# Kernel optimization log

Measured on AMD Instinct MI355X. Metric: run time of the kernel, lower is better.

Reference implementation:

```python
import jax, jax.numpy as jnp
import numpy as np

L, B, T, D, V = 4, 32, 512, 512, 1000


def setup_inputs() -> dict:
    key = jax.random.key(0)
    k0, k1, k2, k3, k4 = jax.random.split(key, 5)
    ids = jax.random.randint(k0, (B, T), 0, V)
    mask = jax.random.randint(k1, (B, T), 0, 2).astype(bool)  # True = valid token
    emb = jax.random.normal(k2, (V, D), dtype=jnp.float32) * 0.1
    W = jax.random.normal(k3, (L, D, 3 * D), dtype=jnp.float32) / np.float32(np.sqrt(D))
    v = jax.random.normal(k4, (L, 2, D), dtype=jnp.float32) * 0.1  # (v_f, v_r) per layer
    b = jnp.zeros((L, 2, D), dtype=jnp.float32)                    # (b_f, b_r) per layer
    return {"ids": ids, "mask": mask, "emb": emb, "W": W, "v": v, "b": b}


def _sru_layer(x, pad, Wl, vf, vr, bf, br):
    # x: [T,B,D] layer input; pad: [T,B,1] bool (True = padded step)
    Tn, Bn, Dn = x.shape
    U = jnp.einsum('tbd,de->tbe', x, Wl).reshape(Tn, Bn, 3, Dn)
    xt, fpre, rpre = U[:, :, 0], U[:, :, 1], U[:, :, 2]

    def step(c, inp):
        xt_t, fp_t, rp_t, x_t, pad_t = inp
        f = jax.nn.sigmoid(fp_t + vf * c + bf)
        r = jax.nn.sigmoid(rp_t + vr * c + br)
        c_new = f * c + (1.0 - f) * xt_t
        h = r * jnp.tanh(c_new) + (1.0 - r) * x_t  # highway (input_size==hidden_size)
        c_out = jnp.where(pad_t, c, c_new)          # padded step: keep state
        h = jnp.where(pad_t, 0.0, h)                # padded step: zero output
        return c_out, h

    c0 = jnp.zeros_like(x[0])  # zero initial hidden state, as in the torch code
    _, h = jax.lax.scan(step, c0, (xt, fpre, rpre, x, pad))
    return h  # [T,B,D]


def reference(ids, mask, emb, W, v, b):
    x = emb[ids]                       # CharEmbedder lookup: [B,T,D]
    x = jnp.transpose(x, (1, 0, 2))    # [T,B,D]  (permute(1,0,2))
    pad = (~mask).T[:, :, None]        # inverted_mask.T -> [T,B,1]
    for l in range(L):
        x = _sru_layer(x, pad, W[l], v[l, 0], v[l, 1], b[l, 0], b[l, 1])
    return jnp.transpose(x, (1, 0, 2))  # back to [B,T,D]
```

## Files before the change

kernel.cpp:

```cpp
#include <hip/hip_runtime.h>
#include <hip/hip_bf16.h>


#define LAYERS 4
#define BB 32
#define TT 512
#define DD 512
#define N3 1536
#define MROWS (TT * BB)
#define WPL ((size_t)DD * N3)
#define SB 32
#define LOG2E 1.4426950408889634f
#define TWOLOG2E 2.8853900817779268f

typedef unsigned short u16;
typedef unsigned int u32;
typedef _Float16 half8 __attribute__((ext_vector_type(8)));
typedef float f32x4 __attribute__((ext_vector_type(4)));

__device__ __forceinline__ float b2f(u16 u) {
  union { unsigned int i; float f; } x;
  x.i = ((unsigned int)u) << 16;
  return x.f;
}
__device__ __forceinline__ u16 f2h(float f) {
  _Float16 h = (_Float16)f;
  return *(u16*)&h;
}
__device__ __forceinline__ float h2f(u16 u) {
  _Float16 h;
  *(u16*)&h = u;
  return (float)h;
}
__device__ __forceinline__ float rcpf(float x) { return __builtin_amdgcn_rcpf(x); }
__device__ __forceinline__ float exp2f_(float x) { return __builtin_amdgcn_exp2f(x); }

__device__ __forceinline__ void async_ld16(const void* g, void* l) {
  __builtin_amdgcn_global_load_lds(
      (const __attribute__((address_space(1))) void*)g,
      (__attribute__((address_space(3))) void*)l, 16, 0, 0);
}
__device__ __forceinline__ void async_ld4(const void* g, void* l) {
  __builtin_amdgcn_global_load_lds(
      (const __attribute__((address_space(1))) void*)g,
      (__attribute__((address_space(3))) void*)l, 4, 0, 0);
}

__global__ void detect_kernel(const u16* __restrict__ emb_u,
                              const int* __restrict__ mask_i,
                              const int* __restrict__ ids_i,
                              int* __restrict__ flags) {
  __shared__ int cnt[3];
  __shared__ int zc;
  int tid = threadIdx.x;
  if (tid < 3) cnt[tid] = 0;
  if (tid == 0) zc = 0;
  __syncthreads();
  int bad = 0, zero_even = 0;
  for (int i = tid; i < 8192; i += 256) {
    u16 u = emb_u[i];
    unsigned e = (u >> 7) & 0xFF;
    if (e >= 0x8F) bad++;
    if ((i & 1) == 0 && u == 0) zero_even++;
  }
  if (bad) atomicAdd(&cnt[0], bad);
  if (zero_even) atomicAdd(&zc, zero_even);
  if (tid < 64) {
    unsigned vv = (unsigned)mask_i[tid];
    if (vv > 1u) atomicAdd(&cnt[1], 1);
  }
  if (tid < 256) {
    if (ids_i[2 * tid + 1] == 0) atomicAdd(&cnt[2], 1);
  }
  __syncthreads();
  if (tid == 0) {
    flags[0] = (cnt[0] > 64 || zc > 3000) ? 1 : 0;
    flags[1] = (cnt[1] > 0) ? 1 : 0;
    flags[2] = (cnt[2] >= 192) ? 1 : 0;
  }
}

__global__ __launch_bounds__(256)
void wprep_kernel(const void* __restrict__ W, u16* __restrict__ W16,
                  const int* __restrict__ flags) {
  __shared__ float tileW[32][33];
  int l = blockIdx.z;
  int k0 = blockIdx.x * 32;
  int n0 = blockIdx.y * 32;
  int tx = threadIdx.x & 31;
  int ty = threadIdx.x >> 5;
  int ff = flags[0];
  const float* Wf = (const float*)W + (size_t)l * WPL;
  const u16* Wb = (const u16*)W + (size_t)l * WPL;
  for (int kk = ty; kk < 32; kk += 8) {
    size_t off = (size_t)(k0 + kk) * N3 + n0 + tx;
    tileW[kk][tx] = ff ? Wf[off] : b2f(Wb[off]);
  }
  __syncthreads();
  u16* outP = W16 + (size_t)l * WPL;
  for (int nn = ty; nn < 32; nn += 8) {
    float x = tileW[tx][nn];
    outP[(size_t)(n0 + nn) * DD + k0 + tx] = f2h(x);
  }
}

__global__ void embed_kernel(const int* __restrict__ ids,
                             const void* __restrict__ emb,
                             u16* __restrict__ X16,
                             const int* __restrict__ flags) {
  int i = blockIdx.x * 256 + threadIdx.x;
  int d = i & (DD - 1);
  int tb = i >> 9;
  int b = tb & (BB - 1);
  int t = tb >> 5;
  int ii = b * TT + t;
  int id = flags[2] ? ids[2 * ii] : ids[ii];
  float val = flags[0] ? ((const float*)emb)[id * DD + d]
                       : b2f(((const u16*)emb)[id * DD + d]);
  X16[i] = f2h(val);
}

__global__ __launch_bounds__(256)
void gemm_kernel(const u16* __restrict__ X16, const u16* __restrict__ W16l,
                 const void* __restrict__ bvec, int layer,
                 const int* __restrict__ flags,
                 u16* __restrict__ U16, int row_base, int chunkM) {
  __shared__ u16 At[128][64];
  __shared__ u16 Bt[128][64];
  const int tid = threadIdx.x;
  const int row0 = blockIdx.x * 128;
  const int col0 = blockIdx.y * 128;
  const int lane = tid & 63, wave = tid >> 6;
  const int wm = (wave >> 1) * 64, wn = (wave & 1) * 64;
  const int m16 = lane & 15, quad = lane >> 4;
  const int isA = (wave < 2);
  const int rbase = (wave & 1) * 64;
  const int srow = lane >> 3;
  const int sseg = (lane & 7) ^ (srow & 7);

  f32x4 acc[4][4];
#pragma unroll
  for (int mi = 0; mi < 4; ++mi)
#pragma unroll
    for (int ni = 0; ni < 4; ++ni)
#pragma unroll
      for (int r = 0; r < 4; ++r) acc[mi][ni][r] = 0.f;

  const u16* srcBase = isA ? X16 : W16l;
  const int gbase = isA ? (row_base + row0 + rbase) : (col0 + rbase);

  for (int kv = 0; kv < 512; kv += 64) {
    __syncthreads();
    {
      const u16* src = srcBase + (size_t)(gbase + srow) * DD + kv + sseg * 8;
      u16(*dst)[64] = isA ? At : Bt;
#pragma unroll
      for (int i = 0; i < 8; ++i)
        async_ld16(src + (size_t)i * 8 * DD, &dst[rbase + i * 8][0]);
    }
    __syncthreads();

    half8 af[2][4], bfr[2][4];
#pragma unroll
    for (int kk = 0; kk < 2; ++kk)
#pragma unroll
      for (int i = 0; i < 4; ++i) {
        int ra = wm + i * 16 + m16;
        af[kk][i] = *(const half8*)&At[ra][((kk * 4 + quad) ^ (ra & 7)) * 8];
        int rb = wn + i * 16 + m16;
        bfr[kk][i] = *(const half8*)&Bt[rb][((kk * 4 + quad) ^ (rb & 7)) * 8];
      }
#pragma unroll
    for (int kk = 0; kk < 2; ++kk)
#pragma unroll
      for (int mi = 0; mi < 4; ++mi)
#pragma unroll
        for (int ni = 0; ni < 4; ++ni)
          acc[mi][ni] = __builtin_amdgcn_mfma_f32_16x16x32_f16(
              af[kk][mi], bfr[kk][ni], acc[mi][ni], 0, 0, 0);
  }

  const int ff = flags[0];
#pragma unroll
  for (int ni = 0; ni < 4; ++ni) {
    int cix = col0 + wn + ni * 16 + m16;
    int p = cix >> 9;
    int dd = cix & 511;
    float bias = 0.f;
    if (p > 0) {
      size_t bo = (size_t)layer * 2 * DD + (size_t)(p - 1) * DD + dd;
      bias = ff ? ((const float*)bvec)[bo] : b2f(((const u16*)bvec)[bo]);
    }
    u16* up = U16 + (size_t)p * chunkM * 512;
#pragma unroll
    for (int mi = 0; mi < 4; ++mi) {
      int r0 = row0 + wm + mi * 16 + quad * 4;
#pragma unroll
      for (int reg = 0; reg < 4; ++reg) {
        float val = acc[mi][ni][reg];
        val = (p == 0) ? val : -(val + bias) * LOG2E;
        up[(size_t)(r0 + reg) * 512 + dd] = f2h(val);
      }
    }
  }
}

template <int EMIT>
__global__ __launch_bounds__(448, 1)
void scan_kernel(const u16* __restrict__ U16, float* __restrict__ X,
                 u16* __restrict__ X16,
                 const void* __restrict__ mask_p, const void* __restrict__ vbase,
                 int layer, const int* __restrict__ flags,
                 float* __restrict__ carry, int t0, int nt, int chunkM) {
  __shared__ u16 bufA[2][2][SB][64];
  __shared__ u16 bufB[3][2][SB][64];
  __shared__ float ring[2][2][SB][64];
  __shared__ int msk[TT];
  const int tid = threadIdx.x;
  const int wave = tid >> 6, lane = tid & 63;
  const int idx0 = blockIdx.x * 64;
  const int b = idx0 >> 9;
  const int d0 = idx0 & 511;
  const int ff = flags[0], fm = flags[1];

  const int* mi_ = (const int*)mask_p + b * TT;
  const unsigned char* mb_ = (const unsigned char*)mask_p + b * TT;
  for (int i = tid; i < nt; i += 448) msk[i] = fm ? (int)mb_[t0 + i] : mi_[t0 + i];

  float vfs = 0.f, vrs = 0.f, c = 0.f;
  {
    int d = d0 + lane;
    size_t voff = (size_t)layer * 2 * DD;
    if (wave == 0) {
      float vf = ff ? ((const float*)vbase)[voff + d]
                    : b2f(((const u16*)vbase)[voff + d]);
      vfs = -vf * LOG2E;
      c = (t0 == 0) ? 0.f : carry[idx0 + lane];
    } else if (wave >= 1 && wave <= 4) {
      float vr = ff ? ((const float*)vbase)[voff + DD + d]
                    : b2f(((const u16*)vbase)[voff + DD + d]);
      vrs = -vr * LOG2E;
    }
  }

  const int nbuf = nt / SB;

  auto ld_pair = [&](const u16* rowS, const u16* rowS1, void* ldst) {
    const u32* a0 = (const u32*)rowS;
    const u32* a1 = (const u32*)rowS1;
    const u32* ga = (lane < 32) ? (a0 + lane) : (a1 + (lane - 32));
    async_ld4(ga, ldst);
  };

  auto produceA = [&](int k) {
    int ph = k & 1, tl = k * SB;
    const u16* p0 = U16 + ((size_t)tl * BB + b) * 512 + d0;
    const u16* p1 = p0 + (size_t)chunkM * 512;
#pragma unroll
    for (int s = 0; s < SB; s += 2)
      ld_pair(p0 + (size_t)s * BB * 512, p0 + (size_t)(s + 1) * BB * 512,
              &bufA[ph][0][s][0]);
#pragma unroll
    for (int s = 0; s < SB; s += 2)
      ld_pair(p1 + (size_t)s * BB * 512, p1 + (size_t)(s + 1) * BB * 512,
              &bufA[ph][1][s][0]);
  };
  auto produceB = [&](int k) {
    int ph = k % 3, tl = k * SB;
    const u16* p2 = U16 + 2 * (size_t)chunkM * 512 + ((size_t)tl * BB + b) * 512 + d0;
    const u16* xb = X16 + ((size_t)(t0 + tl) * BB + b) * DD + d0;
#pragma unroll
    for (int s = 0; s < SB; s += 2)
      ld_pair(p2 + (size_t)s * BB * 512, p2 + (size_t)(s + 1) * BB * 512,
              &bufB[ph][0][s][0]);
#pragma unroll
    for (int s = 0; s < SB; s += 2)
      ld_pair(xb + (size_t)s * BB * DD, xb + (size_t)(s + 1) * BB * DD,
              &bufB[ph][1][s][0]);
  };

  float* Xp = X + (size_t)b * TT * DD + d0 + lane;

  auto hphase = [&](int j, int hw) {
    int phc = j & 1, phb = j % 3;
    int sbase = hw * (SB / 4);
#pragma unroll
    for (int si = 0; si < SB / 4; ++si) {
      int s = sbase + si;
      float cprev = ring[phc][0][s][lane];
      float cn = ring[phc][1][s][lane];
      float rps = h2f(bufB[phb][0][s][lane]);
      float xin = h2f(bufB[phb][1][s][lane]);
      int m = msk[j * SB + s];
      float tr = exp2f_(fmaf(vrs, cprev, rps));
      float r = rcpf(1.f + tr);
      float e2 = exp2f_(cn * TWOLOG2E);
      float th = fmaf(-2.f, rcpf(e2 + 1.f), 1.f);
      float h = fmaf(r, th - xin, xin);
      float hout = (m == 0) ? 0.f : h;
      int tg = t0 + j * SB + s;
      if (EMIT)
        X16[((size_t)tg * BB + b) * DD + d0 + lane] = f2h(hout);
      else
        Xp[(size_t)tg * DD] = hout;
    }
  };

  if (wave == 5) produceA(0);
  if (wave == 6) produceB(0);

  for (int k = 0; k < nbuf; ++k) {
    __syncthreads();
    if (wave == 5) {
      if (k + 1 < nbuf) produceA(k + 1);
    } else if (wave == 6) {
      if (k + 1 < nbuf) produceB(k + 1);
    } else if (wave == 0) {
      int ph = k & 1;
#pragma unroll 8
      for (int s = 0; s < SB; ++s) {
        float xt = h2f(bufA[ph][0][s][lane]);
        float fps = h2f(bufA[ph][1][s][lane]);
        float t = exp2f_(fmaf(vfs, c, fps));
        float f = rcpf(1.f + t);
        float cn = fmaf(f, c - xt, xt);
        ring[ph][0][s][lane] = c;
        ring[ph][1][s][lane] = cn;
        c = (msk[k * SB + s] == 0) ? c : cn;
      }
    } else {
      if (k > 0) hphase(k - 1, wave - 1);
    }
  }
  __syncthreads();
  if (wave >= 1 && wave <= 4) hphase(nbuf - 1, wave - 1);
  if (wave == 0) carry[idx0 + lane] = c;
}

__global__ void sentinel_kernel(float* out) { out[threadIdx.x] = 12345.f; }

extern "C" void kernel_launch(void* const* d_in, const int* in_sizes, int n_in,
                              void* d_out, int out_size, void* d_ws, size_t ws_size,
                              hipStream_t stream) {
  const int* ids = (const int*)d_in[0];
  const void* mask = d_in[1];
  const void* emb = d_in[2];
  const void* W = d_in[3];
  const void* v = d_in[4];
  const void* bp = d_in[5];

  char* ws = (char*)d_ws;
  int* flags = (int*)ws;
  float* carry = (float*)(ws + 4096);
  const size_t offX16 = 69632;
  const size_t offW16 = offX16 + (size_t)MROWS * DD * 2;
  const size_t offU = offW16 + (size_t)LAYERS * WPL * 2;
  const size_t perT = (size_t)BB * N3 * 2;

  const int cand[4] = {512, 256, 128, 64};
  int chunkT = 0;
  for (int i = 0; i < 4; ++i) {
    if (ws_size >= offU + (size_t)cand[i] * perT) { chunkT = cand[i]; break; }
  }
  if (!chunkT) {
    sentinel_kernel<<<1, 256, 0, stream>>>((float*)d_out);
    return;
  }
  const int chunkM = chunkT * BB;

  u16* X16 = (u16*)(ws + offX16);
  u16* W16 = (u16*)(ws + offW16);
  u16* U16 = (u16*)(ws + offU);
  float* X = (float*)d_out;

  detect_kernel<<<1, 256, 0, stream>>>((const u16*)emb, (const int*)mask,
                                       (const int*)ids, flags);
  wprep_kernel<<<dim3(16, 48, 4), 256, 0, stream>>>(W, W16, flags);
  embed_kernel<<<MROWS * DD / 256, 256, 0, stream>>>(ids, emb, X16, flags);

  int nch = TT / chunkT;
  for (int l = 0; l < LAYERS; ++l) {
    const u16* W16l = W16 + (size_t)l * WPL;
    for (int ch = 0; ch < nch; ++ch) {
      int t0 = ch * chunkT;
      dim3 g(chunkT * BB / 128, N3 / 128);
      gemm_kernel<<<g, 256, 0, stream>>>(X16, W16l, bp, l, flags, U16,
                                         t0 * BB, chunkM);
      if (l < LAYERS - 1)
        scan_kernel<1><<<BB * DD / 64, 448, 0, stream>>>(U16, X, X16, mask, v, l,
                                                         flags, carry, t0, chunkT,
                                                         chunkM);
      else
        scan_kernel<0><<<BB * DD / 64, 448, 0, stream>>>(U16, X, X16, mask, v, l,
                                                         flags, carry, t0, chunkT,
                                                         chunkM);
    }
  }
}
```

Baseline: 353.0 us.

## Rewrite GEMM with 256x256 tiles, 8 waves and double-buffered async LDS pipeline

The projection GEMM moves from 128x128 tiles with 4 waves and two barriers per K step to 256x256 tiles with 8 waves. Global-to-LDS async loads are double-buffered and prefetched several stages ahead, with manual vmcnt waits and raw s_barrier calls, and MFMA priority is raised. Workgroup IDs are remapped across groups of 8 so neighbouring blocks share operands in cache. The aim is more reuse per tile and load latency hidden behind MFMA work. The costs are fewer blocks (risk of idle CUs when chunkM is small), hand-tuned wait counts that must match the issue order, and an nblk that is assumed divisible by 8.

```diff
diff --git a/kernel.cpp b/kernel.cpp
--- a/kernel.cpp
+++ b/kernel.cpp
@@ -17,6 +17,9 @@
 typedef unsigned int u32;
 typedef _Float16 half8 __attribute__((ext_vector_type(8)));
 typedef float f32x4 __attribute__((ext_vector_type(4)));
+
+#define SBAR() asm volatile("s_barrier" ::: "memory")
+#define WAITVM(n) asm volatile("s_waitcnt vmcnt(" n ")" ::: "memory")
 
 __device__ __forceinline__ float b2f(u16 u) {
   union { unsigned int i; float f; } x;
@@ -120,88 +123,121 @@
   X16[i] = f2h(val);
 }
 
-__global__ __launch_bounds__(256)
+__global__ __launch_bounds__(512, 2)
 void gemm_kernel(const u16* __restrict__ X16, const u16* __restrict__ W16l,
                  const void* __restrict__ bvec, int layer,
                  const int* __restrict__ flags,
-                 u16* __restrict__ U16, int row_base, int chunkM) {
-  __shared__ u16 At[128][64];
-  __shared__ u16 Bt[128][64];
+                 u16* __restrict__ U16, int row_base, int chunkM, int nblk) {
+  __shared__ u16 lds[2][2][2][8192];
   const int tid = threadIdx.x;
-  const int row0 = blockIdx.x * 128;
-  const int col0 = blockIdx.y * 128;
   const int lane = tid & 63, wave = tid >> 6;
-  const int wm = (wave >> 1) * 64, wn = (wave & 1) * 64;
+  const int wm = wave >> 2, wn = wave & 3;
   const int m16 = lane & 15, quad = lane >> 4;
-  const int isA = (wave < 2);
-  const int rbase = (wave & 1) * 64;
-  const int srow = lane >> 3;
-  const int sseg = (lane & 7) ^ (srow & 7);
-
-  f32x4 acc[4][4];
-#pragma unroll
-  for (int mi = 0; mi < 4; ++mi)
+
+  const int orig = blockIdx.x;
+  const int wg = (orig & 7) * (nblk >> 3) + (orig >> 3);
+  const int mt = wg / 6, nt = wg - mt * 6;
+
+  const int arow0 = row_base + mt * 256;
+  const int bcol0 = nt * 256;
+
+  const int srow = lane >> 2;
+  const int sq = (lane & 3) ^ (srow & 3);
+  const u16* pa = X16 + (size_t)(arow0 + wave * 32 + srow) * DD + sq * 8;
+  const u16* pb = W16l + (size_t)(bcol0 + wave * 32 + srow) * DD + sq * 8;
+  const int ldsblk = wave * 2 * 512;
+
+  auto stage = [&](int s) {
+    const int ts = s >> 2, hi = s & 3;
+    const int mat = hi & 1, kk = hi >> 1, db = ts & 1;
+    const u16* src = (mat ? pb : pa) + ts * 64 + kk * 32;
+    u16* dst = &lds[db][mat][kk][ldsblk];
+    async_ld16(src, dst);
+    async_ld16(src + (size_t)16 * DD, dst + 512);
+  };
+
+  f32x4 acc[8][4];
+#pragma unroll
+  for (int mi = 0; mi < 8; ++mi)
 #pragma unroll
     for (int ni = 0; ni < 4; ++ni)
 #pragma unroll
       for (int r = 0; r < 4; ++r) acc[mi][ni][r] = 0.f;
 
-  const u16* srcBase = isA ? X16 : W16l;
-  const int gbase = isA ? (row_base + row0 + rbase) : (col0 + rbase);
-
-  for (int kv = 0; kv < 512; kv += 64) {
-    __syncthreads();
-    {
-      const u16* src = srcBase + (size_t)(gbase + srow) * DD + kv + sseg * 8;
-      u16(*dst)[64] = isA ? At : Bt;
-#pragma unroll
-      for (int i = 0; i < 8; ++i)
-        async_ld16(src + (size_t)i * 8 * DD, &dst[rbase + i * 8][0]);
-    }
-    __syncthreads();
-
-    half8 af[2][4], bfr[2][4];
-#pragma unroll
-    for (int kk = 0; kk < 2; ++kk)
-#pragma unroll
-      for (int i = 0; i < 4; ++i) {
-        int ra = wm + i * 16 + m16;
-        af[kk][i] = *(const half8*)&At[ra][((kk * 4 + quad) ^ (ra & 7)) * 8];
-        int rb = wn + i * 16 + m16;
-        bfr[kk][i] = *(const half8*)&Bt[rb][((kk * 4 + quad) ^ (rb & 7)) * 8];
+#pragma unroll
+  for (int s = 0; s < 6; ++s) stage(s);
+  WAITVM("4");
+  SBAR();
+
+  const int loff = m16 * 32 + (quad ^ (lane & 3)) * 8;
+  half8 bf[4];
+
+  for (int t = 0; t < 8; ++t) {
+    const int db = t & 1;
+#pragma unroll
+    for (int p = 0; p < 4; ++p) {
+      const int kk = p >> 1;
+      const int mh = (p == 1 || p == 2) ? 1 : 0;
+      half8 af[4];
+      const u16* Ab = &lds[db][0][kk][(wm * 8 + mh * 4) * 512 + loff];
+#pragma unroll
+      for (int i = 0; i < 4; ++i) af[i] = *(const half8*)(Ab + i * 512);
+      if (p == 0 || p == 2) {
+        const u16* Bb = &lds[db][1][kk][wn * 4 * 512 + loff];
+#pragma unroll
+        for (int i = 0; i < 4; ++i) bf[i] = *(const half8*)(Bb + i * 512);
       }
-#pragma unroll
-    for (int kk = 0; kk < 2; ++kk)
+      const int s = t * 4 + p + 6;
+      if (s < 32) stage(s);
+      SBAR();
+      __builtin_amdgcn_s_setprio(1);
 #pragma unroll
       for (int mi = 0; mi < 4; ++mi)
 #pragma unroll
         for (int ni = 0; ni < 4; ++ni)
-          acc[mi][ni] = __builtin_amdgcn_mfma_f32_16x16x32_f16(
-              af[kk][mi], bfr[kk][ni], acc[mi][ni], 0, 0, 0);
+          acc[mh * 4 + mi][ni] = __builtin_amdgcn_mfma_f32_16x16x32_f16(
+              af[mi], bf[ni], acc[mh * 4 + mi][ni], 0, 0, 0);
+      __builtin_amdgcn_s_setprio(0);
+      if (p == 3) {
+        if (t == 6) WAITVM("0");
+        else WAITVM("4");
+      }
+      SBAR();
+    }
   }
 
   const int ff = flags[0];
-#pragma unroll
-  for (int ni = 0; ni < 4; ++ni) {
-    int cix = col0 + wn + ni * 16 + m16;
-    int p = cix >> 9;
-    int dd = cix & 511;
-    float bias = 0.f;
-    if (p > 0) {
-      size_t bo = (size_t)layer * 2 * DD + (size_t)(p - 1) * DD + dd;
-      bias = ff ? ((const float*)bvec)[bo] : b2f(((const u16*)bvec)[bo]);
-    }
-    u16* up = U16 + (size_t)p * chunkM * 512;
-#pragma unroll
-    for (int mi = 0; mi < 4; ++mi) {
-      int r0 = row0 + wm + mi * 16 + quad * 4;
+  const int pl = nt >> 1;
+  const int dd0 = (nt & 1) * 256;
+  u16* up = U16 + (size_t)pl * chunkM * 512;
+  const int r0 = mt * 256 + wm * 128 + quad * 4;
+  const int c0 = dd0 + wn * 64 + m16;
+  if (pl == 0) {
+#pragma unroll
+    for (int mi = 0; mi < 8; ++mi)
 #pragma unroll
       for (int reg = 0; reg < 4; ++reg) {
-        float val = acc[mi][ni][reg];
-        val = (p == 0) ? val : -(val + bias) * LOG2E;
-        up[(size_t)(r0 + reg) * 512 + dd] = f2h(val);
+        size_t rb = (size_t)(r0 + mi * 16 + reg) * 512 + c0;
+#pragma unroll
+        for (int ni = 0; ni < 4; ++ni)
+          up[rb + ni * 16] = f2h(acc[mi][ni][reg]);
       }
-    }
+  } else {
+    float bias[4];
+#pragma unroll
+    for (int ni = 0; ni < 4; ++ni) {
+      size_t bo = (size_t)layer * 2 * DD + (size_t)(pl - 1) * DD + c0 + ni * 16;
+      bias[ni] = ff ? ((const float*)bvec)[bo] : b2f(((const u16*)bvec)[bo]);
+    }
+#pragma unroll
+    for (int mi = 0; mi < 8; ++mi)
+#pragma unroll
+      for (int reg = 0; reg < 4; ++reg) {
+        size_t rb = (size_t)(r0 + mi * 16 + reg) * 512 + c0;
+#pragma unroll
+        for (int ni = 0; ni < 4; ++ni)
+          up[rb + ni * 16] = f2h(-(acc[mi][ni][reg] + bias[ni]) * LOG2E);
+      }
   }
 }
 
@@ -383,9 +419,9 @@
     const u16* W16l = W16 + (size_t)l * WPL;
     for (int ch = 0; ch < nch; ++ch) {
       int t0 = ch * chunkT;
-      dim3 g(chunkT * BB / 128, N3 / 128);
-      gemm_kernel<<<g, 256, 0, stream>>>(X16, W16l, bp, l, flags, U16,
-                                         t0 * BB, chunkM);
+      int nblk = (chunkM / 256) * 6;
+      gemm_kernel<<<nblk, 512, 0, stream>>>(X16, W16l, bp, l, flags, U16,
+                                            t0 * BB, chunkM, nblk);
       if (l < LAYERS - 1)
         scan_kernel<1><<<BB * DD / 64, 448, 0, stream>>>(U16, X, X16, mask, v, l,
                                                          flags, carry, t0, chunkT,
```

Result: slower. 361.2 us (+2.3%).
